# Performance work log

Measured on AMD Instinct MI355X. Metric: run time of the kernel, lower is better.

The kernel has to match this reference:

```python
import jax, jax.numpy as jnp
import numpy as np
from jax.scipy.special import erf

B, S, D, H, F = 2, 2048, 1024, 16, 4096
EPS = 1e-5


def setup_inputs() -> dict:
    key = jax.random.key(0)
    ks = jax.random.split(key, 7)
    s = 0.02  # init scale so attention logits stay in a sane range
    return {
        "x": jax.random.normal(ks[0], (B, S, D), jnp.float32),
        "wq": jax.random.normal(ks[1], (D, D), jnp.float32) * s,
        "wk": jax.random.normal(ks[2], (D, D), jnp.float32) * s,
        "wv": jax.random.normal(ks[3], (D, D), jnp.float32) * s,
        "wo": jax.random.normal(ks[4], (D, D), jnp.float32) * s,
        "w1": jax.random.normal(ks[5], (F, D), jnp.float32) * s,
        "w2": jax.random.normal(ks[6], (D, F), jnp.float32) * s,
        "g1": jnp.ones((D,), jnp.float32),
        "g2": jnp.ones((D,), jnp.float32),
    }


def _rmsnorm(x, g):
    return x / jnp.sqrt(jnp.mean(x * x, axis=-1, keepdims=True) + EPS) * g


def _gelu_exact(x):
    # 0.5 * x * (1 + erf(x / sqrt(2)))
    return 0.5 * x * (1.0 + erf(x * (1.0 / np.sqrt(2.0).astype(np.float32))))


def reference(x, wq, wk, wv, wo, w1, w2, g1, g2):
    b, s, d = x.shape
    dk = d // H
    # --- attention sublayer (pre-RMSNorm) ---
    h = _rmsnorm(x, g1)
    # Linear(bias=False): y = h @ W.T; split heads -> [b, H, s, dk]
    q = (h @ wq.T).reshape(b, s, H, dk).transpose(0, 2, 1, 3)
    k = (h @ wk.T).reshape(b, s, H, dk).transpose(0, 2, 1, 3)
    v = (h @ wv.T).reshape(b, s, H, dk).transpose(0, 2, 1, 3)
    scores = jnp.einsum('bhqd,bhkd->bhqk', q, k) / jnp.sqrt(jnp.float32(dk))
    causal = jnp.triu(jnp.ones((s, s), bool), 1)  # True above diagonal -> masked
    scores = jnp.where(causal, -jnp.inf, scores)
    attn = jax.nn.softmax(scores, axis=-1)
    o = jnp.einsum('bhqk,bhkd->bhqd', attn, v)
    o = o.transpose(0, 2, 1, 3).reshape(b, s, d) @ wo.T
    x = x + o
    # --- FFN sublayer (pre-RMSNorm, exact-erf GELU) ---
    h2 = _rmsnorm(x, g2)
    f = _gelu_exact(h2 @ w1.T) @ w2.T
    return x + f
```

## Files before the change

### kernel.cpp

```cpp
#include <hip/hip_runtime.h>
#include <hip/hip_bf16.h>
#include <math.h>

#define B_   2
#define S_   2048
#define D_   1024
#define H_   16
#define DK_  64
#define F_   4096
#define NTOK (B_ * S_)

typedef __bf16 bf16x8 __attribute__((ext_vector_type(8)));
typedef float  f32x4  __attribute__((ext_vector_type(4)));

__device__ __forceinline__ unsigned short bf16r(float f) {
  unsigned u = __builtin_bit_cast(unsigned, f);
  u += 0x7fffu + ((u >> 16) & 1u);
  return (unsigned short)(u >> 16);
}

__device__ __forceinline__ void gload_lds16(const void* g, void* l) {
  __builtin_amdgcn_global_load_lds(
      (__attribute__((address_space(1))) void*)g,
      (__attribute__((address_space(3))) void*)l, 16, 0, 0);
}

__device__ __forceinline__ unsigned lds_off(void* p) {
  return (unsigned)(size_t)(__attribute__((address_space(3))) void*)p;
}
__device__ __forceinline__ bf16x8 ds_read16(unsigned a) {
  bf16x8 r;
  asm volatile("ds_read_b128 %0, %1" : "=v"(r) : "v"(a));
  return r;
}
__device__ __forceinline__ void ds_write32(unsigned a, unsigned v) {
  asm volatile("ds_write_b32 %0, %1" : : "v"(a), "v"(v));
}
__device__ __forceinline__ void ds_write16b(unsigned a, unsigned v) {
  asm volatile("ds_write_b16 %0, %1" : : "v"(a), "v"(v));
}
__device__ __forceinline__ float fexp2(float x) {
  float r;
  asm volatile("v_exp_f32 %0, %1\n\ts_nop 0" : "=v"(r) : "v"(x));
  return r;
}
__device__ __forceinline__ unsigned cvt_pk_bf16(float lo, float hi) {
  unsigned r;
  asm volatile("v_cvt_pk_bf16_f32 %0, %1, %2" : "=v"(r) : "v"(lo), "v"(hi));
  return r;
}

__device__ __forceinline__ float gelu_fast(float x) {
  float y = 0.7978845608f * x * (1.0f + 0.044715f * x * x);
  float e = fexp2(2.885390082f * y);
  float t = 1.0f - 2.0f / (e + 1.0f);
  return 0.5f * x * (1.0f + t);
}

#define QSCL 0.18033688f

struct CvtArgs {
  const float* src[6];
  unsigned short* dst[6];
  int start[7];
};
__global__ __launch_bounds__(256) void cvt_all_kernel(CvtArgs a) {
  int i = blockIdx.x * blockDim.x + threadIdx.x;
  if (i >= a.start[6]) return;
  int k = 0;
#pragma unroll
  for (int j = 1; j < 6; ++j)
    if (i >= a.start[j]) k = j;
  int off = i - a.start[k];
  float4 v = reinterpret_cast<const float4*>(a.src[k])[off];
  ushort4 o;
  o.x = bf16r(v.x); o.y = bf16r(v.y); o.z = bf16r(v.z); o.w = bf16r(v.w);
  reinterpret_cast<ushort4*>(a.dst[k])[off] = o;
}

__global__ __launch_bounds__(256) void rmsnorm_kernel(
    const float* __restrict__ x, const float* __restrict__ g,
    unsigned short* __restrict__ out) {
  int row = blockIdx.x;
  int t = threadIdx.x, lane = t & 63, w = t >> 6;
  float4 v = reinterpret_cast<const float4*>(x + (size_t)row * D_)[t];
  float ss = v.x * v.x + v.y * v.y + v.z * v.z + v.w * v.w;
#pragma unroll
  for (int d = 1; d < 64; d <<= 1) ss += __shfl_xor(ss, d);
  __shared__ float red[4];
  if (lane == 0) red[w] = ss;
  __syncthreads();
  float tot = red[0] + red[1] + red[2] + red[3];
  float rstd = rsqrtf(tot * (1.0f / D_) + 1e-5f);
  float4 gv = reinterpret_cast<const float4*>(g)[t];
  ushort4 o;
  o.x = bf16r(v.x * rstd * gv.x);
  o.y = bf16r(v.y * rstd * gv.y);
  o.z = bf16r(v.z * rstd * gv.z);
  o.w = bf16r(v.w * rstd * gv.w);
  reinterpret_cast<ushort4*>(out + (size_t)row * D_)[t] = o;
}

__device__ __forceinline__ void store_tile_coalesced(
    const f32x4 (&acc)[4][4], unsigned ew, int lane, int lg, int ln,
    unsigned short* __restrict__ dst, size_t stride, int rowbase, int colbase,
    bool gelu, float scl) {
#pragma unroll
  for (int m = 0; m < 4; ++m)
#pragma unroll
    for (int n = 0; n < 4; ++n)
#pragma unroll
      for (int j = 0; j < 4; ++j) {
        int lrow = lg * 4 + m * 16 + j;
        int lcol = n * 16 + ln;
        int g = (lcol >> 3) ^ (lrow & 7);
        float v = acc[m][n][j];
        if (gelu) v = gelu_fast(v);
        ds_write16b(ew + (unsigned)((lrow * 64 + g * 8 + (lcol & 7)) * 2),
                    (unsigned)bf16r(v * scl));
      }
  asm volatile("s_waitcnt lgkmcnt(0)");
  __builtin_amdgcn_sched_barrier(0);
  bf16x8 cv[8];
#pragma unroll
  for (int i = 0; i < 8; ++i) {
    int lrow = i * 8 + (lane >> 3);
    int g = (lane & 7) ^ (lrow & 7);
    cv[i] = ds_read16(ew + (unsigned)((lrow * 64 + g * 8) * 2));
  }
  asm volatile("s_waitcnt lgkmcnt(0)");
  __builtin_amdgcn_sched_barrier(0);
#pragma unroll
  for (int i = 0; i < 8; ++i) {
    int lrow = i * 8 + (lane >> 3);
    *reinterpret_cast<bf16x8*>(
        &dst[(size_t)(rowbase + lrow) * stride + colbase + (lane & 7) * 8]) = cv[i];
  }
}

__global__ __launch_bounds__(512, 4) void ffn1_gemm(
    const unsigned short* __restrict__ A, const unsigned short* __restrict__ Bw,
    int M, int N, int K, unsigned short* __restrict__ outB) {
  constexpr int BUFU = 12288;
  __shared__ __attribute__((aligned(16))) unsigned short lds[3 * BUFU];
  const int t = threadIdx.x, lane = t & 63, w = t >> 6;
  const int wm = w >> 1, wn = w & 1;
  const int lg = lane >> 4, ln = lane & 15;

  const int gx = gridDim.x;
  int bid = blockIdx.y * gx + blockIdx.x;
  int xcd = bid & 7, c = bid >> 3;
  int RX = gx >> 2, RY = gridDim.y >> 1;
  int bx = (xcd & 3) * RX + (c % RX);
  int by = (xcd >> 2) * RY + (c / RX);
  const int m0 = by * 256, n0 = bx * 128;

  const int nt = K >> 5;

  auto stage = [&](int tile) {
    int buf = tile % 3;
    const int k0 = tile << 5;
    unsigned short* la = &lds[buf * BUFU];
    unsigned short* lb = la + 8192;
#pragma unroll
    for (int i = 0; i < 2; ++i) {
      int g = i * 512 + t;
      int Ln = g >> 3, p = g & 7, u = p ^ (Ln & 7);
      int row = 2 * Ln + (u >> 2), cg = u & 3;
      gload_lds16(A + (size_t)(m0 + row) * K + k0 + cg * 8, &la[g * 8]);
    }
    {
      int Ln = t >> 3, p = t & 7, u = p ^ (Ln & 7);
      int row = 2 * Ln + (u >> 2), cg = u & 3;
      gload_lds16(Bw + (size_t)(n0 + row) * K + k0 + cg * 8, &lb[t * 8]);
    }
  };

  stage(0);
  stage(1);

  const unsigned base0 = lds_off(lds);
  unsigned offA[4], offB[4];
#pragma unroll
  for (int m = 0; m < 4; ++m) {
    int r = wm * 64 + m * 16 + ln;
    int Ln = r >> 1, p = ((r & 1) * 4 + lg) ^ (Ln & 7);
    offA[m] = (unsigned)((Ln * 64 + p * 8) * 2);
  }
#pragma unroll
  for (int n = 0; n < 4; ++n) {
    int r = wn * 64 + n * 16 + ln;
    int Ln = r >> 1, p = ((r & 1) * 4 + lg) ^ (Ln & 7);
    offB[n] = (unsigned)(16384 + (Ln * 64 + p * 8) * 2);
  }

  f32x4 acc[4][4] = {};

  for (int tile = 0; tile < nt; ++tile) {
    if (tile + 1 < nt) { asm volatile("s_waitcnt vmcnt(3)"); }
    else               { asm volatile("s_waitcnt vmcnt(0)"); }
    __builtin_amdgcn_sched_barrier(0);
    __builtin_amdgcn_s_barrier();
    const unsigned bb = base0 + (unsigned)((tile % 3) * (BUFU * 2));
    bf16x8 af[4], bf0, bf1;
#pragma unroll
    for (int m = 0; m < 4; ++m) af[m] = ds_read16(bb + offA[m]);
    bf0 = ds_read16(bb + offB[0]);
    bf1 = ds_read16(bb + offB[1]);
    if (tile + 2 < nt) stage(tile + 2);
    asm volatile("s_waitcnt lgkmcnt(0)");
    __builtin_amdgcn_sched_barrier(0);
    __builtin_amdgcn_s_setprio(1);
#pragma unroll
    for (int m = 0; m < 4; ++m) {
      acc[m][0] = __builtin_amdgcn_mfma_f32_16x16x32_bf16(af[m], bf0, acc[m][0], 0, 0, 0);
      acc[m][1] = __builtin_amdgcn_mfma_f32_16x16x32_bf16(af[m], bf1, acc[m][1], 0, 0, 0);
    }
    __builtin_amdgcn_s_setprio(0);
    bf0 = ds_read16(bb + offB[2]);
    bf1 = ds_read16(bb + offB[3]);
    asm volatile("s_waitcnt lgkmcnt(0)");
    __builtin_amdgcn_sched_barrier(0);
    __builtin_amdgcn_s_setprio(1);
#pragma unroll
    for (int m = 0; m < 4; ++m) {
      acc[m][2] = __builtin_amdgcn_mfma_f32_16x16x32_bf16(af[m], bf0, acc[m][2], 0, 0, 0);
      acc[m][3] = __builtin_amdgcn_mfma_f32_16x16x32_bf16(af[m], bf1, acc[m][3], 0, 0, 0);
    }
    __builtin_amdgcn_s_setprio(0);
  }

  __builtin_amdgcn_s_barrier();
  const unsigned ew = base0 + (unsigned)(w * 8192);
  store_tile_coalesced(acc, ew, lane, lg, ln, outB, (size_t)N,
                       m0 + wm * 64, n0 + wn * 64, true, 1.0f);
}

__global__ __launch_bounds__(256, 3) void qkv_gemm(
    const unsigned short* __restrict__ A, const unsigned short* __restrict__ Bw,
    int M, int N, int K,
    unsigned short* __restrict__ outB, unsigned short* __restrict__ outB2,
    unsigned short* __restrict__ outB3) {
  constexpr int BUFU = 8192;
  __shared__ __attribute__((aligned(16))) unsigned short lds[3 * BUFU];
  const int t = threadIdx.x, lane = t & 63, w = t >> 6;
  const int wm = w >> 1, wn = w & 1;
  const int lg = lane >> 4, ln = lane & 15;

  const int gx = gridDim.x;
  int bid = blockIdx.y * gx + blockIdx.x;
  int xcd = bid & 7, c = bid >> 3;
  int RX = gx >> 2, RY = gridDim.y >> 1;
  int bx = (xcd & 3) * RX + (c % RX);
  int by = (xcd >> 2) * RY + (c / RX);
  const int m0 = by * 128, n0 = bx * 128;

  const int nt = K >> 5;

  auto stage = [&](int tile) {
    int buf = tile % 3;
    const int k0 = tile << 5;
    unsigned short* la = &lds[buf * BUFU];
    unsigned short* lb = la + 4096;
#pragma unroll
    for (int i = 0; i < 2; ++i) {
      int g = i * 256 + t;
      int Ln = g >> 3, p = g & 7, u = p ^ (Ln & 7);
      int row = 2 * Ln + (u >> 2), cg = u & 3;
      gload_lds16(A + (size_t)(m0 + row) * K + k0 + cg * 8, &la[g * 8]);
    }
#pragma unroll
    for (int i = 0; i < 2; ++i) {
      int g = i * 256 + t;
      int Ln = g >> 3, p = g & 7, u = p ^ (Ln & 7);
      int row = 2 * Ln + (u >> 2), cg = u & 3;
      gload_lds16(Bw + (size_t)(n0 + row) * K + k0 + cg * 8, &lb[g * 8]);
    }
  };

  stage(0);
  stage(1);

  const unsigned base0 = lds_off(lds);
  unsigned offA[4], offB[4];
#pragma unroll
  for (int m = 0; m < 4; ++m) {
    int r = wm * 64 + m * 16 + ln;
    int Ln = r >> 1, p = ((r & 1) * 4 + lg) ^ (Ln & 7);
    offA[m] = (unsigned)((Ln * 64 + p * 8) * 2);
  }
#pragma unroll
  for (int n = 0; n < 4; ++n) {
    int r = wn * 64 + n * 16 + ln;
    int Ln = r >> 1, p = ((r & 1) * 4 + lg) ^ (Ln & 7);
    offB[n] = (unsigned)(8192 + (Ln * 64 + p * 8) * 2);
  }

  f32x4 acc[4][4] = {};

  for (int tile = 0; tile < nt; ++tile) {
    if (tile + 1 < nt) { asm volatile("s_waitcnt vmcnt(4)"); }
    else               { asm volatile("s_waitcnt vmcnt(0)"); }
    __builtin_amdgcn_sched_barrier(0);
    __builtin_amdgcn_s_barrier();
    const unsigned bb = base0 + (unsigned)((tile % 3) * (BUFU * 2));
    bf16x8 af[4], bf[4];
#pragma unroll
    for (int m = 0; m < 4; ++m) af[m] = ds_read16(bb + offA[m]);
#pragma unroll
    for (int n = 0; n < 4; ++n) bf[n] = ds_read16(bb + offB[n]);
    if (tile + 2 < nt) stage(tile + 2);
    asm volatile("s_waitcnt lgkmcnt(0)");
    __builtin_amdgcn_sched_barrier(0);
    __builtin_amdgcn_s_setprio(1);
#pragma unroll
    for (int m = 0; m < 4; ++m)
#pragma unroll
      for (int n = 0; n < 4; ++n)
        acc[m][n] = __builtin_amdgcn_mfma_f32_16x16x32_bf16(af[m], bf[n], acc[m][n], 0, 0, 0);
    __builtin_amdgcn_s_setprio(0);
  }

  __builtin_amdgcn_s_barrier();
  const unsigned ew = base0 + (unsigned)(w * 8192);
  const int col0 = n0 + wn * 64;
  const int rowbase = m0 + wm * 64;
  if (col0 < 2 * D_) {
    const float scl = (col0 < D_) ? QSCL : 1.0f;
    unsigned short* dst = (col0 < D_) ? outB : outB2;
    const int cb = (col0 < D_) ? col0 : col0 - D_;
    store_tile_coalesced(acc, ew, lane, lg, ln, dst, (size_t)D_,
                         rowbase, cb, false, scl);
  } else {
    const int cb = col0 - 2 * D_;
    const int bb2 = rowbase >> 11;
    const int s0base = rowbase & (S_ - 1);
#pragma unroll
    for (int m = 0; m < 4; ++m) {
#pragma unroll
      for (int n = 0; n < 4; ++n) {
        int col = cb + n * 16 + ln;
        ushort4 pk;
        pk.x = bf16r(acc[m][n][0]);
        pk.y = bf16r(acc[m][n][1]);
        pk.z = bf16r(acc[m][n][2]);
        pk.w = bf16r(acc[m][n][3]);
        *reinterpret_cast<ushort4*>(
            &outB3[((size_t)(bb2 * D_) + col) * S_ + s0base + lg * 4 + m * 16]) = pk;
      }
    }
  }
}

__device__ __forceinline__ void gemm128_body(
    const unsigned short* __restrict__ A, const unsigned short* __restrict__ Bw,
    int M, int N, int K,
    const float* __restrict__ resid, float* __restrict__ outF) {
  constexpr int BUFU = 256 * 32;
  __shared__ __attribute__((aligned(16))) unsigned short lds[4 * BUFU];
  const int t = threadIdx.x, lane = t & 63, w = t >> 6;
  const int wm = w >> 2, wn = w & 3;
  const int lg = lane >> 4, ln = lane & 15;

  const int gx = gridDim.x;
  int bid = blockIdx.y * gx + blockIdx.x;
  int RX = gx >> 2, RY = gridDim.y >> 1;
  int xcd = bid & 7, c = bid >> 3;
  int bx = (xcd & 3) * RX + (c % RX);
  int by = (xcd >> 2) * RY + (c / RX);
  const int m0 = by * 128, n0 = bx * 128;

  const int nt = K >> 5;

  auto stage = [&](int tile) {
    const int buf = tile & 3;
    const int k0 = tile << 5;
    unsigned short* la = &lds[buf * BUFU];
    unsigned short* lb = la + 4096;
    int Ln = t >> 3, p = t & 7, u = p ^ (Ln & 7);
    int row = 2 * Ln + (u >> 2), cg = u & 3;
    gload_lds16(A + (size_t)(m0 + row) * K + k0 + cg * 8, &la[t * 8]);
    gload_lds16(Bw + (size_t)(n0 + row) * K + k0 + cg * 8, &lb[t * 8]);
  };

  stage(0);
  if (nt > 1) stage(1);
  if (nt > 2) stage(2);

  const unsigned base0 = lds_off(lds);
  unsigned offA[4], offB[2];
#pragma unroll
  for (int m = 0; m < 4; ++m) {
    int r = wm * 64 + m * 16 + ln;
    int Ln = r >> 1, p = ((r & 1) * 4 + lg) ^ (Ln & 7);
    offA[m] = (unsigned)((Ln * 64 + p * 8) * 2);
  }
#pragma unroll
  for (int n = 0; n < 2; ++n) {
    int r = wn * 32 + n * 16 + ln;
    int Ln = r >> 1, p = ((r & 1) * 4 + lg) ^ (Ln & 7);
    offB[n] = (unsigned)(8192 + (Ln * 64 + p * 8) * 2);
  }

  f32x4 acc[4][2] = {};

  for (int tile = 0; tile < nt; ++tile) {
    const int rem = nt - 1 - tile;
    if (rem >= 2)      { asm volatile("s_waitcnt vmcnt(4)"); }
    else if (rem == 1) { asm volatile("s_waitcnt vmcnt(2)"); }
    else               { asm volatile("s_waitcnt vmcnt(0)"); }
    __builtin_amdgcn_sched_barrier(0);
    __builtin_amdgcn_s_barrier();
    const unsigned bb = base0 + (unsigned)((tile & 3) * (BUFU * 2));
    bf16x8 af[4], bf[2];
#pragma unroll
    for (int m = 0; m < 4; ++m) af[m] = ds_read16(bb + offA[m]);
#pragma unroll
    for (int n = 0; n < 2; ++n) bf[n] = ds_read16(bb + offB[n]);
    if (tile + 3 < nt) stage(tile + 3);
    asm volatile("s_waitcnt lgkmcnt(0)");
    __builtin_amdgcn_sched_barrier(0);
    __builtin_amdgcn_s_setprio(1);
#pragma unroll
    for (int m = 0; m < 4; ++m)
#pragma unroll
      for (int n = 0; n < 2; ++n)
        acc[m][n] = __builtin_amdgcn_mfma_f32_16x16x32_bf16(af[m], bf[n], acc[m][n], 0, 0, 0);
    __builtin_amdgcn_s_setprio(0);
  }

  const int rbase = m0 + wm * 64 + lg * 4;
  const int cbase = n0 + wn * 32 + ln;
#pragma unroll
  for (int m = 0; m < 4; ++m) {
#pragma unroll
    for (int n = 0; n < 2; ++n) {
      int col = cbase + n * 16;
#pragma unroll
      for (int j = 0; j < 4; ++j) {
        int row = rbase + m * 16 + j;
        outF[(size_t)row * N + col] = acc[m][n][j] + resid[(size_t)row * N + col];
      }
    }
  }
}

__global__ __launch_bounds__(512, 4) void wo_gemm(
    const unsigned short* __restrict__ A, const unsigned short* __restrict__ Bw,
    int M, int N, int K, const float* __restrict__ resid, float* __restrict__ outF) {
  gemm128_body(A, Bw, M, N, K, resid, outF);
}
__global__ __launch_bounds__(512, 4) void ffn2_gemm(
    const unsigned short* __restrict__ A, const unsigned short* __restrict__ Bw,
    int M, int N, int K, const float* __restrict__ resid, float* __restrict__ outF) {
  gemm128_body(A, Bw, M, N, K, resid, outF);
}

#define PV_ISSUE(c, pa, v0, v1, v2, v3) do {                                   \
  unsigned cg_ = (unsigned)(((((c) * 4) + lg) ^ ln) & 15);                     \
  pa = ds_read16(pbase + (unsigned)(ln * 256) + cg_ * 16);                     \
  v0 = ds_read16(vb + (unsigned)((0 * 16 + ln) * 256) + cg_ * 16);             \
  v1 = ds_read16(vb + (unsigned)((1 * 16 + ln) * 256) + cg_ * 16);             \
  v2 = ds_read16(vb + (unsigned)((2 * 16 + ln) * 256) + cg_ * 16);             \
  v3 = ds_read16(vb + (unsigned)((3 * 16 + ln) * 256) + cg_ * 16);             \
} while (0)

#define PV_MFMA(pa, v0, v1, v2, v3) do {                                       \
  oacc[0] = __builtin_amdgcn_mfma_f32_16x16x32_bf16(pa, v0, oacc[0], 0, 0, 0); \
  oacc[1] = __builtin_amdgcn_mfma_f32_16x16x32_bf16(pa, v1, oacc[1], 0, 0, 0); \
  oacc[2] = __builtin_amdgcn_mfma_f32_16x16x32_bf16(pa, v2, oacc[2], 0, 0, 0); \
  oacc[3] = __builtin_amdgcn_mfma_f32_16x16x32_bf16(pa, v3, oacc[3], 0, 0, 0); \
} while (0)

__global__ __launch_bounds__(256, 2) void attn_kernel(
    const unsigned short* __restrict__ qg, const unsigned short* __restrict__ kg,
    const unsigned short* __restrict__ vt, unsigned short* __restrict__ og) {
  __shared__ __attribute__((aligned(16))) unsigned short Kl[2][8192];
  __shared__ __attribute__((aligned(16))) unsigned short Vl[2][8192];
  __shared__ __attribute__((aligned(16))) unsigned short Pl[4][2048];
  const int t = threadIdx.x, lane = t & 63, w = t >> 6;
  const int lg = lane >> 4, ln = lane & 15;

  int bid = blockIdx.x;
  int nl = (bid & 7) * 64 + (bid >> 3);
  int bh = nl >> 4, pi = nl & 15;
  int b = bh >> 4, h = bh & 15;

  const unsigned kbase = lds_off(&Kl[0][0]);
  const unsigned vbase = lds_off(&Vl[0][0]);
  const unsigned pbase = lds_off(&Pl[w][0]);

  auto runq = [&](int qtile, bool first) {
    const int q0 = qtile * 64;
    const int qw = q0 + w * 16;
    const int nt = (q0 >> 7) + 1;

    bf16x8 aq[2];
    {
      const unsigned short* qp =
          qg + (size_t)(b * S_ + qw + ln) * D_ + h * DK_ + lg * 8;
      aq[0] = *reinterpret_cast<const bf16x8*>(qp);
      aq[1] = *reinterpret_cast<const bf16x8*>(qp + 32);
    }
    asm volatile("" : : "v"(aq[0]), "v"(aq[1]));

    float mr = -1e30f, lr = 0.f;
    f32x4 oacc[4] = {};

    auto stage = [&](int kt) {
      const int buf = kt & 1;
      const int kv0 = kt * 128;
#pragma unroll
      for (int i = 0; i < 4; ++i) {
        int g = i * 256 + t;
        int row = g >> 3, cg = g & 7, sg = cg ^ (row & 7);
        gload_lds16(kg + (size_t)(b * S_ + kv0 + row) * D_ + h * DK_ + sg * 8,
                    &Kl[buf][g * 8]);
      }
#pragma unroll
      for (int i = 0; i < 4; ++i) {
        int g = i * 256 + t;
        int row = g >> 4, cg = g & 15, sg = cg ^ (row & 15);
        gload_lds16(vt + (size_t)(b * D_ + h * DK_ + row) * S_ + kv0 + sg * 8,
                    &Vl[buf][g * 8]);
      }
    };

    if (!first) __builtin_amdgcn_s_barrier();
    stage(0);

    auto ctile = [&](int kt, bool dm) {
      const unsigned kb = kbase + (unsigned)((kt & 1) * 16384);
      const unsigned vb = vbase + (unsigned)((kt & 1) * 16384);
      f32x4 sc[8] = {};
      bf16x8 kf[8], kf2[8];
#pragma unroll
      for (int n = 0; n < 8; ++n) {
        int r = n * 16 + ln;
        int cg0 = lg ^ (r & 7);
        kf[n] = ds_read16(kb + (unsigned)((r * 128 + cg0 * 16)));
      }
#pragma unroll
      for (int n = 0; n < 8; ++n) {
        int r = n * 16 + ln;
        int cg1 = (4 + lg) ^ (r & 7);
        kf2[n] = ds_read16(kb + (unsigned)((r * 128 + cg1 * 16)));
      }
      if (!dm) stage(kt + 1);
      asm volatile("s_waitcnt lgkmcnt(8)");
      __builtin_amdgcn_sched_barrier(0);
#pragma unroll
      for (int n = 0; n < 8; ++n)
        sc[n] = __builtin_amdgcn_mfma_f32_16x16x32_bf16(kf[n], aq[0], sc[n], 0, 0, 0);
      asm volatile("s_waitcnt lgkmcnt(0)");
      __builtin_amdgcn_sched_barrier(0);
#pragma unroll
      for (int n = 0; n < 8; ++n)
        sc[n] = __builtin_amdgcn_mfma_f32_16x16x32_bf16(kf2[n], aq[1], sc[n], 0, 0, 0);
      if (dm) {
        const int kv0 = kt * 128;
        const int qi = qw + ln;
#pragma unroll
        for (int n = 0; n < 8; ++n)
#pragma unroll
          for (int j = 0; j < 4; ++j)
            if ((kv0 + n * 16 + lg * 4 + j) > qi) sc[n][j] = -1e30f;
      }
      float mx = -1e30f;
#pragma unroll
      for (int n = 0; n < 8; ++n) {
        float a = fmaxf(fmaxf(sc[n][0], sc[n][1]), fmaxf(sc[n][2], sc[n][3]));
        mx = fmaxf(mx, a);
      }
      mx = fmaxf(mx, __shfl_xor(mx, 16));
      mx = fmaxf(mx, __shfl_xor(mx, 32));
      float mn = fmaxf(mr, mx);
      float ps = 0.f;
#pragma unroll
      for (int n = 0; n < 8; ++n)
#pragma unroll
        for (int j = 0; j < 4; ++j) {
          float p = fexp2(sc[n][j] - mn);
          sc[n][j] = p;
          ps += p;
        }
      if (__all(mx <= mr)) {
        lr += ps;
      } else {
        float sf = fexp2(mr - mn);
        mr = mn;
        lr = lr * sf + ps;
#pragma unroll
        for (int j = 0; j < 4; ++j) {
          float sfj = __shfl(sf, lg * 4 + j);
#pragma unroll
          for (int f = 0; f < 4; ++f) oacc[f][j] *= sfj;
        }
      }
#pragma unroll
      for (int n = 0; n < 8; ++n) {
        int kvc = n * 16 + lg * 4;
        int gsw = ((kvc >> 3) ^ ln) & 15;
        unsigned pa_addr = pbase + (unsigned)(ln * 256 + gsw * 16 + (kvc & 7) * 2);
        ds_write32(pa_addr, cvt_pk_bf16(sc[n][0], sc[n][1]));
        ds_write32(pa_addr + 4, cvt_pk_bf16(sc[n][2], sc[n][3]));
      }
      asm volatile("s_waitcnt lgkmcnt(0)");
      __builtin_amdgcn_sched_barrier(0);
      bf16x8 paA, vA0, vA1, vA2, vA3, paB, vB0, vB1, vB2, vB3;
      PV_ISSUE(0, paA, vA0, vA1, vA2, vA3);
      PV_ISSUE(1, paB, vB0, vB1, vB2, vB3);
      asm volatile("s_waitcnt lgkmcnt(5)");
      __builtin_amdgcn_sched_barrier(0);
      PV_MFMA(paA, vA0, vA1, vA2, vA3);
      PV_ISSUE(2, paA, vA0, vA1, vA2, vA3);
      asm volatile("s_waitcnt lgkmcnt(5)");
      __builtin_amdgcn_sched_barrier(0);
      PV_MFMA(paB, vB0, vB1, vB2, vB3);
      PV_ISSUE(3, paB, vB0, vB1, vB2, vB3);
      asm volatile("s_waitcnt lgkmcnt(5)");
      __builtin_amdgcn_sched_barrier(0);
      PV_MFMA(paA, vA0, vA1, vA2, vA3);
      asm volatile("s_waitcnt lgkmcnt(0)");
      __builtin_amdgcn_sched_barrier(0);
      PV_MFMA(paB, vB0, vB1, vB2, vB3);
    };

    for (int kt = 0; kt < nt - 1; ++kt) {
      asm volatile("s_waitcnt vmcnt(0)");
      __builtin_amdgcn_sched_barrier(0);
      __builtin_amdgcn_s_barrier();
      ctile(kt, false);
    }
    asm volatile("s_waitcnt vmcnt(0)");
    __builtin_amdgcn_sched_barrier(0);
    __builtin_amdgcn_s_barrier();
    ctile(nt - 1, true);

    lr += __shfl_xor(lr, 16);
    lr += __shfl_xor(lr, 32);
#pragma unroll
    for (int j = 0; j < 4; ++j) {
      float lj = __shfl(lr, lg * 4 + j);
      float inv = 1.0f / lj;
      int row = b * S_ + qw + lg * 4 + j;
#pragma unroll
      for (int f = 0; f < 4; ++f)
        og[(size_t)row * D_ + h * DK_ + f * 16 + ln] = bf16r(oacc[f][j] * inv);
    }
  };

  runq(31 - pi, true);
  runq(pi, false);
}

extern "C" void kernel_launch(void* const* d_in, const int* in_sizes, int n_in,
                              void* d_out, int out_size, void* d_ws, size_t ws_size,
                              hipStream_t stream) {
  const float* x  = (const float*)d_in[0];
  const float* wq = (const float*)d_in[1];
  const float* wk = (const float*)d_in[2];
  const float* wv = (const float*)d_in[3];
  const float* wo = (const float*)d_in[4];
  const float* w1 = (const float*)d_in[5];
  const float* w2 = (const float*)d_in[6];
  const float* g1 = (const float*)d_in[7];
  const float* g2 = (const float*)d_in[8];
  float* out = (float*)d_out;

  char* ws = (char*)d_ws;
  const size_t MB = 1024 * 1024;
  unsigned short* wqkv_b = (unsigned short*)(ws + 0 * MB);
  unsigned short* wo_b   = (unsigned short*)(ws + 6 * MB);
  unsigned short* w1_b   = (unsigned short*)(ws + 8 * MB);
  unsigned short* w2_b   = (unsigned short*)(ws + 16 * MB);
  unsigned short* h_b    = (unsigned short*)(ws + 24 * MB);
  unsigned short* q_b    = (unsigned short*)(ws + 32 * MB);
  unsigned short* k_b    = (unsigned short*)(ws + 40 * MB);
  unsigned short* vt_b   = (unsigned short*)(ws + 48 * MB);
  unsigned short* o_b    = (unsigned short*)(ws + 56 * MB);
  float*          x1     = (float*)(ws + 64 * MB);
  unsigned short* mid    = (unsigned short*)(ws + 80 * MB);

  CvtArgs ca;
  ca.src[0] = wq; ca.dst[0] = wqkv_b;
  ca.src[1] = wk; ca.dst[1] = wqkv_b + (size_t)D_ * D_;
  ca.src[2] = wv; ca.dst[2] = wqkv_b + (size_t)2 * D_ * D_;
  ca.src[3] = wo; ca.dst[3] = wo_b;
  ca.src[4] = w1; ca.dst[4] = w1_b;
  ca.src[5] = w2; ca.dst[5] = w2_b;
  int q4 = D_ * D_ / 4, f4 = F_ * D_ / 4;
  ca.start[0] = 0;
  ca.start[1] = q4;
  ca.start[2] = 2 * q4;
  ca.start[3] = 3 * q4;
  ca.start[4] = 4 * q4;
  ca.start[5] = 4 * q4 + f4;
  ca.start[6] = 4 * q4 + 2 * f4;
  cvt_all_kernel<<<(ca.start[6] + 255) / 256, 256, 0, stream>>>(ca);

  rmsnorm_kernel<<<NTOK, 256, 0, stream>>>(x, g1, h_b);

  qkv_gemm<<<dim3(3 * D_ / 128, NTOK / 128), dim3(256), 0, stream>>>(
      h_b, wqkv_b, NTOK, 3 * D_, D_, q_b, k_b, vt_b);

  attn_kernel<<<dim3(512), dim3(256), 0, stream>>>(q_b, k_b, vt_b, o_b);

  wo_gemm<<<dim3(D_ / 128, NTOK / 128), dim3(512), 0, stream>>>(
      o_b, wo_b, NTOK, D_, D_, x, x1);

  rmsnorm_kernel<<<NTOK, 256, 0, stream>>>(x1, g2, h_b);

  ffn1_gemm<<<dim3(F_ / 128, NTOK / 256), dim3(512), 0, stream>>>(
      h_b, w1_b, NTOK, F_, D_, mid);

  ffn2_gemm<<<dim3(D_ / 128, NTOK / 128), dim3(512), 0, stream>>>(
      mid, w2_b, NTOK, D_, F_, x1, out);
}
```

Before: 206.7 us.

## Share a two-tile-per-iteration 128x128 GEMM body between QKV and FFN1

Replaces the separate ffn1 kernel (256x128 tile, 512 threads) with a shared templated 128x128 body that runs 256 threads over a 4-slot LDS ring. Each iteration processes two K-tiles, waiting on global loads and the barrier once per pair rather than once per tile. The aim is to halve synchronisation overhead and overlap the second tile's LDS reads with the first tile's MFMAs. In exchange the waitcnt becomes vmcnt(0), so the prefetch depth is shallower, LDS use grows, occupancy hints drop to 2, and ffn1 loses A-tile reuse because its tile shrinks.

```diff
diff --git a/kernel.cpp b/kernel.cpp
--- a/kernel.cpp
+++ b/kernel.cpp
@@ -138,111 +138,14 @@
   }
 }
 
-__global__ __launch_bounds__(512, 4) void ffn1_gemm(
-    const unsigned short* __restrict__ A, const unsigned short* __restrict__ Bw,
-    int M, int N, int K, unsigned short* __restrict__ outB) {
-  constexpr int BUFU = 12288;
-  __shared__ __attribute__((aligned(16))) unsigned short lds[3 * BUFU];
-  const int t = threadIdx.x, lane = t & 63, w = t >> 6;
-  const int wm = w >> 1, wn = w & 1;
-  const int lg = lane >> 4, ln = lane & 15;
-
-  const int gx = gridDim.x;
-  int bid = blockIdx.y * gx + blockIdx.x;
-  int xcd = bid & 7, c = bid >> 3;
-  int RX = gx >> 2, RY = gridDim.y >> 1;
-  int bx = (xcd & 3) * RX + (c % RX);
-  int by = (xcd >> 2) * RY + (c / RX);
-  const int m0 = by * 256, n0 = bx * 128;
-
-  const int nt = K >> 5;
-
-  auto stage = [&](int tile) {
-    int buf = tile % 3;
-    const int k0 = tile << 5;
-    unsigned short* la = &lds[buf * BUFU];
-    unsigned short* lb = la + 8192;
-#pragma unroll
-    for (int i = 0; i < 2; ++i) {
-      int g = i * 512 + t;
-      int Ln = g >> 3, p = g & 7, u = p ^ (Ln & 7);
-      int row = 2 * Ln + (u >> 2), cg = u & 3;
-      gload_lds16(A + (size_t)(m0 + row) * K + k0 + cg * 8, &la[g * 8]);
-    }
-    {
-      int Ln = t >> 3, p = t & 7, u = p ^ (Ln & 7);
-      int row = 2 * Ln + (u >> 2), cg = u & 3;
-      gload_lds16(Bw + (size_t)(n0 + row) * K + k0 + cg * 8, &lb[t * 8]);
-    }
-  };
-
-  stage(0);
-  stage(1);
-
-  const unsigned base0 = lds_off(lds);
-  unsigned offA[4], offB[4];
-#pragma unroll
-  for (int m = 0; m < 4; ++m) {
-    int r = wm * 64 + m * 16 + ln;
-    int Ln = r >> 1, p = ((r & 1) * 4 + lg) ^ (Ln & 7);
-    offA[m] = (unsigned)((Ln * 64 + p * 8) * 2);
-  }
-#pragma unroll
-  for (int n = 0; n < 4; ++n) {
-    int r = wn * 64 + n * 16 + ln;
-    int Ln = r >> 1, p = ((r & 1) * 4 + lg) ^ (Ln & 7);
-    offB[n] = (unsigned)(16384 + (Ln * 64 + p * 8) * 2);
-  }
-
-  f32x4 acc[4][4] = {};
-
-  for (int tile = 0; tile < nt; ++tile) {
-    if (tile + 1 < nt) { asm volatile("s_waitcnt vmcnt(3)"); }
-    else               { asm volatile("s_waitcnt vmcnt(0)"); }
-    __builtin_amdgcn_sched_barrier(0);
-    __builtin_amdgcn_s_barrier();
-    const unsigned bb = base0 + (unsigned)((tile % 3) * (BUFU * 2));
-    bf16x8 af[4], bf0, bf1;
-#pragma unroll
-    for (int m = 0; m < 4; ++m) af[m] = ds_read16(bb + offA[m]);
-    bf0 = ds_read16(bb + offB[0]);
-    bf1 = ds_read16(bb + offB[1]);
-    if (tile + 2 < nt) stage(tile + 2);
-    asm volatile("s_waitcnt lgkmcnt(0)");
-    __builtin_amdgcn_sched_barrier(0);
-    __builtin_amdgcn_s_setprio(1);
-#pragma unroll
-    for (int m = 0; m < 4; ++m) {
-      acc[m][0] = __builtin_amdgcn_mfma_f32_16x16x32_bf16(af[m], bf0, acc[m][0], 0, 0, 0);
-      acc[m][1] = __builtin_amdgcn_mfma_f32_16x16x32_bf16(af[m], bf1, acc[m][1], 0, 0, 0);
-    }
-    __builtin_amdgcn_s_setprio(0);
-    bf0 = ds_read16(bb + offB[2]);
-    bf1 = ds_read16(bb + offB[3]);
-    asm volatile("s_waitcnt lgkmcnt(0)");
-    __builtin_amdgcn_sched_barrier(0);
-    __builtin_amdgcn_s_setprio(1);
-#pragma unroll
-    for (int m = 0; m < 4; ++m) {
-      acc[m][2] = __builtin_amdgcn_mfma_f32_16x16x32_bf16(af[m], bf0, acc[m][2], 0, 0, 0);
-      acc[m][3] = __builtin_amdgcn_mfma_f32_16x16x32_bf16(af[m], bf1, acc[m][3], 0, 0, 0);
-    }
-    __builtin_amdgcn_s_setprio(0);
-  }
-
-  __builtin_amdgcn_s_barrier();
-  const unsigned ew = base0 + (unsigned)(w * 8192);
-  store_tile_coalesced(acc, ew, lane, lg, ln, outB, (size_t)N,
-                       m0 + wm * 64, n0 + wn * 64, true, 1.0f);
-}
-
-__global__ __launch_bounds__(256, 3) void qkv_gemm(
+template <int EPI>
+__device__ __forceinline__ void gemm_pair_body(
     const unsigned short* __restrict__ A, const unsigned short* __restrict__ Bw,
     int M, int N, int K,
     unsigned short* __restrict__ outB, unsigned short* __restrict__ outB2,
     unsigned short* __restrict__ outB3) {
   constexpr int BUFU = 8192;
-  __shared__ __attribute__((aligned(16))) unsigned short lds[3 * BUFU];
+  __shared__ __attribute__((aligned(16))) unsigned short lds[4 * BUFU];
   const int t = threadIdx.x, lane = t & 63, w = t >> 6;
   const int wm = w >> 1, wn = w & 1;
   const int lg = lane >> 4, ln = lane & 15;
@@ -258,7 +161,7 @@
   const int nt = K >> 5;
 
   auto stage = [&](int tile) {
-    int buf = tile % 3;
+    int buf = tile & 3;
     const int k0 = tile << 5;
     unsigned short* la = &lds[buf * BUFU];
     unsigned short* lb = la + 4096;
@@ -298,18 +201,32 @@
 
   f32x4 acc[4][4] = {};
 
-  for (int tile = 0; tile < nt; ++tile) {
-    if (tile + 1 < nt) { asm volatile("s_waitcnt vmcnt(4)"); }
-    else               { asm volatile("s_waitcnt vmcnt(0)"); }
+  for (int tp = 0; tp < nt; tp += 2) {
+    asm volatile("s_waitcnt vmcnt(0)");
     __builtin_amdgcn_sched_barrier(0);
     __builtin_amdgcn_s_barrier();
-    const unsigned bb = base0 + (unsigned)((tile % 3) * (BUFU * 2));
-    bf16x8 af[4], bf[4];
-#pragma unroll
-    for (int m = 0; m < 4; ++m) af[m] = ds_read16(bb + offA[m]);
-#pragma unroll
-    for (int n = 0; n < 4; ++n) bf[n] = ds_read16(bb + offB[n]);
-    if (tile + 2 < nt) stage(tile + 2);
+    const unsigned bb0 = base0 + (unsigned)((tp & 3) * (BUFU * 2));
+    const unsigned bb1 = base0 + (unsigned)(((tp + 1) & 3) * (BUFU * 2));
+    bf16x8 af[4], bf[4], af2[4], bf2[4];
+#pragma unroll
+    for (int m = 0; m < 4; ++m) af[m] = ds_read16(bb0 + offA[m]);
+#pragma unroll
+    for (int n = 0; n < 4; ++n) bf[n] = ds_read16(bb0 + offB[n]);
+#pragma unroll
+    for (int m = 0; m < 4; ++m) af2[m] = ds_read16(bb1 + offA[m]);
+#pragma unroll
+    for (int n = 0; n < 4; ++n) bf2[n] = ds_read16(bb1 + offB[n]);
+    if (tp + 2 < nt) stage(tp + 2);
+    if (tp + 3 < nt) stage(tp + 3);
+    asm volatile("s_waitcnt lgkmcnt(8)");
+    __builtin_amdgcn_sched_barrier(0);
+    __builtin_amdgcn_s_setprio(1);
+#pragma unroll
+    for (int m = 0; m < 4; ++m)
+#pragma unroll
+      for (int n = 0; n < 4; ++n)
+        acc[m][n] = __builtin_amdgcn_mfma_f32_16x16x32_bf16(af[m], bf[n], acc[m][n], 0, 0, 0);
+    __builtin_amdgcn_s_setprio(0);
     asm volatile("s_waitcnt lgkmcnt(0)");
     __builtin_amdgcn_sched_barrier(0);
     __builtin_amdgcn_s_setprio(1);
@@ -317,7 +234,7 @@
     for (int m = 0; m < 4; ++m)
 #pragma unroll
       for (int n = 0; n < 4; ++n)
-        acc[m][n] = __builtin_amdgcn_mfma_f32_16x16x32_bf16(af[m], bf[n], acc[m][n], 0, 0, 0);
+        acc[m][n] = __builtin_amdgcn_mfma_f32_16x16x32_bf16(af2[m], bf2[n], acc[m][n], 0, 0, 0);
     __builtin_amdgcn_s_setprio(0);
   }
 
@@ -325,31 +242,47 @@
   const unsigned ew = base0 + (unsigned)(w * 8192);
   const int col0 = n0 + wn * 64;
   const int rowbase = m0 + wm * 64;
-  if (col0 < 2 * D_) {
-    const float scl = (col0 < D_) ? QSCL : 1.0f;
-    unsigned short* dst = (col0 < D_) ? outB : outB2;
-    const int cb = (col0 < D_) ? col0 : col0 - D_;
-    store_tile_coalesced(acc, ew, lane, lg, ln, dst, (size_t)D_,
-                         rowbase, cb, false, scl);
+  if (EPI == 1) {
+    store_tile_coalesced(acc, ew, lane, lg, ln, outB, (size_t)N,
+                         rowbase, col0, true, 1.0f);
   } else {
-    const int cb = col0 - 2 * D_;
-    const int bb2 = rowbase >> 11;
-    const int s0base = rowbase & (S_ - 1);
-#pragma unroll
-    for (int m = 0; m < 4; ++m) {
-#pragma unroll
-      for (int n = 0; n < 4; ++n) {
-        int col = cb + n * 16 + ln;
-        ushort4 pk;
-        pk.x = bf16r(acc[m][n][0]);
-        pk.y = bf16r(acc[m][n][1]);
-        pk.z = bf16r(acc[m][n][2]);
-        pk.w = bf16r(acc[m][n][3]);
-        *reinterpret_cast<ushort4*>(
-            &outB3[((size_t)(bb2 * D_) + col) * S_ + s0base + lg * 4 + m * 16]) = pk;
+    if (col0 < 2 * D_) {
+      const float scl = (col0 < D_) ? QSCL : 1.0f;
+      unsigned short* dst = (col0 < D_) ? outB : outB2;
+      const int cb = (col0 < D_) ? col0 : col0 - D_;
+      store_tile_coalesced(acc, ew, lane, lg, ln, dst, (size_t)D_,
+                           rowbase, cb, false, scl);
+    } else {
+      const int cb = col0 - 2 * D_;
+      const int bb2 = rowbase >> 11;
+      const int s0base = rowbase & (S_ - 1);
+#pragma unroll
+      for (int m = 0; m < 4; ++m) {
+#pragma unroll
+        for (int n = 0; n < 4; ++n) {
+          int col = cb + n * 16 + ln;
+          ushort4 pk;
+          pk.x = bf16r(acc[m][n][0]);
+          pk.y = bf16r(acc[m][n][1]);
+          pk.z = bf16r(acc[m][n][2]);
+          pk.w = bf16r(acc[m][n][3]);
+          *reinterpret_cast<ushort4*>(
+              &outB3[((size_t)(bb2 * D_) + col) * S_ + s0base + lg * 4 + m * 16]) = pk;
+        }
       }
     }
   }
+}
+
+__global__ __launch_bounds__(256, 2) void qkv_gemm(
+    const unsigned short* __restrict__ A, const unsigned short* __restrict__ Bw,
+    int M, int N, int K, unsigned short* o1, unsigned short* o2, unsigned short* o3) {
+  gemm_pair_body<4>(A, Bw, M, N, K, o1, o2, o3);
+}
+__global__ __launch_bounds__(256, 2) void ffn1_gemm(
+    const unsigned short* __restrict__ A, const unsigned short* __restrict__ Bw,
+    int M, int N, int K, unsigned short* o1) {
+  gemm_pair_body<1>(A, Bw, M, N, K, o1, nullptr, nullptr);
 }
 
 __device__ __forceinline__ void gemm128_body(
@@ -711,7 +644,7 @@
 
   rmsnorm_kernel<<<NTOK, 256, 0, stream>>>(x1, g2, h_b);
 
-  ffn1_gemm<<<dim3(F_ / 128, NTOK / 256), dim3(512), 0, stream>>>(
+  ffn1_gemm<<<dim3(F_ / 128, NTOK / 128), dim3(256), 0, stream>>>(
       h_b, w1_b, NTOK, F_, D_, mid);
 
   ffn2_gemm<<<dim3(D_ / 128, NTOK / 128), dim3(512), 0, stream>>>(
```

Result: no change. 207.0 us (+0.1%).

## Process two K-tiles per iteration in QKV GEMM with four LDS buffers

Applied to the files above, without the earlier changes.

Restructures the qkv_gemm main loop so that each iteration reads two K-tiles from LDS and stages the next two tiles into a 4-deep ring of LDS buffers. This halves the number of block barriers and full vmcnt waits per K-step, and lets the second tile's LDS reads overlap the first tile's MFMAs. In exchange, LDS per block grows to 64KB and launch bounds drop from 3 to 2 blocks per CU, which lowers occupancy. It also waits for all outstanding global loads at the top of each iteration, which may expose more memory latency than the earlier vmcnt(4) scheme.

```diff
diff --git a/kernel.cpp b/kernel.cpp
--- a/kernel.cpp
+++ b/kernel.cpp
@@ -236,13 +236,13 @@
                        m0 + wm * 64, n0 + wn * 64, true, 1.0f);
 }
 
-__global__ __launch_bounds__(256, 3) void qkv_gemm(
+__global__ __launch_bounds__(256, 2) void qkv_gemm(
     const unsigned short* __restrict__ A, const unsigned short* __restrict__ Bw,
     int M, int N, int K,
     unsigned short* __restrict__ outB, unsigned short* __restrict__ outB2,
     unsigned short* __restrict__ outB3) {
   constexpr int BUFU = 8192;
-  __shared__ __attribute__((aligned(16))) unsigned short lds[3 * BUFU];
+  __shared__ __attribute__((aligned(16))) unsigned short lds[4 * BUFU];
   const int t = threadIdx.x, lane = t & 63, w = t >> 6;
   const int wm = w >> 1, wn = w & 1;
   const int lg = lane >> 4, ln = lane & 15;
@@ -258,7 +258,7 @@
   const int nt = K >> 5;
 
   auto stage = [&](int tile) {
-    int buf = tile % 3;
+    int buf = tile & 3;
     const int k0 = tile << 5;
     unsigned short* la = &lds[buf * BUFU];
     unsigned short* lb = la + 4096;
@@ -298,19 +298,24 @@
 
   f32x4 acc[4][4] = {};
 
-  for (int tile = 0; tile < nt; ++tile) {
-    if (tile + 1 < nt) { asm volatile("s_waitcnt vmcnt(4)"); }
-    else               { asm volatile("s_waitcnt vmcnt(0)"); }
+  for (int tp = 0; tp < nt; tp += 2) {
+    asm volatile("s_waitcnt vmcnt(0)");
     __builtin_amdgcn_sched_barrier(0);
     __builtin_amdgcn_s_barrier();
-    const unsigned bb = base0 + (unsigned)((tile % 3) * (BUFU * 2));
-    bf16x8 af[4], bf[4];
-#pragma unroll
-    for (int m = 0; m < 4; ++m) af[m] = ds_read16(bb + offA[m]);
-#pragma unroll
-    for (int n = 0; n < 4; ++n) bf[n] = ds_read16(bb + offB[n]);
-    if (tile + 2 < nt) stage(tile + 2);
-    asm volatile("s_waitcnt lgkmcnt(0)");
+    const unsigned bb0 = base0 + (unsigned)((tp & 3) * (BUFU * 2));
+    const unsigned bb1 = base0 + (unsigned)(((tp + 1) & 3) * (BUFU * 2));
+    bf16x8 af[4], bf[4], af2[4], bf2[4];
+#pragma unroll
+    for (int m = 0; m < 4; ++m) af[m] = ds_read16(bb0 + offA[m]);
+#pragma unroll
+    for (int n = 0; n < 4; ++n) bf[n] = ds_read16(bb0 + offB[n]);
+#pragma unroll
+    for (int m = 0; m < 4; ++m) af2[m] = ds_read16(bb1 + offA[m]);
+#pragma unroll
+    for (int n = 0; n < 4; ++n) bf2[n] = ds_read16(bb1 + offB[n]);
+    if (tp + 2 < nt) stage(tp + 2);
+    if (tp + 3 < nt) stage(tp + 3);
+    asm volatile("s_waitcnt lgkmcnt(8)");
     __builtin_amdgcn_sched_barrier(0);
     __builtin_amdgcn_s_setprio(1);
 #pragma unroll
@@ -318,6 +323,15 @@
 #pragma unroll
       for (int n = 0; n < 4; ++n)
         acc[m][n] = __builtin_amdgcn_mfma_f32_16x16x32_bf16(af[m], bf[n], acc[m][n], 0, 0, 0);
+    __builtin_amdgcn_s_setprio(0);
+    asm volatile("s_waitcnt lgkmcnt(0)");
+    __builtin_amdgcn_sched_barrier(0);
+    __builtin_amdgcn_s_setprio(1);
+#pragma unroll
+    for (int m = 0; m < 4; ++m)
+#pragma unroll
+      for (int n = 0; n < 4; ++n)
+        acc[m][n] = __builtin_amdgcn_mfma_f32_16x16x32_bf16(af2[m], bf2[n], acc[m][n], 0, 0, 0);
     __builtin_amdgcn_s_setprio(0);
   }
 
```

Result: no change. 206.2 us (-0.2%).
